# Kernel tuning notes

Measured on AMD Instinct MI355X. Metric: run time of the kernel, lower is better.

## Reference

```python
import jax, jax.numpy as jnp
import numpy as np

B, SEQ, DIM = 2, 2048, 1024
HEADS, DIM_HEAD = 16, 64
INNER = HEADS * DIM_HEAD
SCALE = DIM_HEAD ** -0.5


def rotate_half(x):
    # pair consecutive dims (d r) with r=2: (x1, x2) -> (-x2, x1)
    xp = x.reshape(*x.shape[:-1], -1, 2)
    x1, x2 = xp[..., 0], xp[..., 1]
    return jnp.stack((-x2, x1), axis=-1).reshape(x.shape)


def apply_rotary_emb(freqs, t):
    # freqs: [n, rot_dim] angles; t: [b, h, n, d]
    rot_dim = freqs.shape[-1]
    t_rot, t_pass = t[..., :rot_dim], t[..., rot_dim:]
    t_rot = t_rot * jnp.cos(freqs) + rotate_half(t_rot) * jnp.sin(freqs)
    return jnp.concatenate([t_rot, t_pass], axis=-1)


def setup_inputs() -> dict:
    key = jax.random.key(0)
    ks = jax.random.split(key, 4)
    x = jax.random.normal(ks[0], (B, SEQ, DIM), dtype=jnp.float32)
    mask = jnp.ones((B, SEQ), dtype=bool)
    rotary_pos_emb = jax.random.uniform(ks[1], (SEQ, DIM_HEAD), dtype=jnp.float32)
    Wqkv = jax.random.normal(ks[2], (DIM, 3 * INNER), dtype=jnp.float32) * 0.02
    Wout = jax.random.normal(ks[3], (INNER, DIM), dtype=jnp.float32) * 0.02
    bout = jnp.zeros((DIM,), dtype=jnp.float32)
    return {"x": x, "mask": mask, "rotary_pos_emb": rotary_pos_emb,
            "Wqkv": Wqkv, "Wout": Wout, "bout": bout}


def reference(x, mask, rotary_pos_emb, Wqkv, Wout, bout):
    b, n, _ = x.shape
    qkv = x @ Wqkv                                   # [b, n, 3*inner]
    q, k, v = jnp.split(qkv, 3, axis=-1)

    def to_heads(t):
        return t.reshape(b, n, HEADS, DIM_HEAD).transpose(0, 2, 1, 3)  # [b,h,n,d]

    q, k, v = to_heads(q), to_heads(k), to_heads(v)
    freqs = rotary_pos_emb[:n, :]
    # NB: original applies rotary to q, k AND v
    q = apply_rotary_emb(freqs, q)
    k = apply_rotary_emb(freqs, k)
    v = apply_rotary_emb(freqs, v)
    q = q * SCALE

    dots = jnp.einsum('bhid,bhjd->bhij', q, k)       # [b,h,n,n]
    mask_value = -jnp.finfo(dots.dtype).max
    pad = mask[:, None, None, :]                     # [b,1,1,n] keep where True
    dots = jnp.where(pad, dots, mask_value)
    idx = jnp.arange(n)
    causal = idx[None, :] > idx[:, None]             # j >= i + (j-i+1) with i==j==n
    dots = jnp.where(causal[None, None], mask_value, dots)

    attn = jax.nn.softmax(dots, axis=-1)
    out = jnp.einsum('bhij,bhjd->bhid', attn, v)     # [b,h,n,d]
    out = out.transpose(0, 2, 1, 3).reshape(b, n, INNER)
    return out @ Wout + bout
```

## Files before the change

### kernel.cpp

```cpp
#include <hip/hip_runtime.h>
#include <hip/hip_bf16.h>
#include <stdint.h>

#define DEVI __device__ __forceinline__

typedef __bf16 bf16x8 __attribute__((ext_vector_type(8)));
typedef float f32x4 __attribute__((ext_vector_type(4)));
typedef float f32x16 __attribute__((ext_vector_type(16)));

static constexpr int SEQ = 2048;
static constexpr int DIM = 1024;
static constexpr int HEADS = 16;
static constexpr int NQKV = 3072;
static constexpr int MROWS = 4096;
static constexpr float QSCALE = 0.125f;
static constexpr float LOG2E = 1.4426950408889634f;

DEVI unsigned short f2bf(float f) {
  unsigned int u = __builtin_bit_cast(unsigned int, f);
  u += 0x7FFFu + ((u >> 16) & 1u);
  return (unsigned short)(u >> 16);
}

DEVI bf16x8 ld8(const unsigned short* p) {
  return __builtin_bit_cast(bf16x8, *(const uint4*)p);
}

DEVI f32x4 mfma16(bf16x8 a, bf16x8 b, f32x4 c) {
  return __builtin_amdgcn_mfma_f32_16x16x32_bf16(a, b, c, 0, 0, 0);
}

DEVI f32x16 mfma32(bf16x8 a, bf16x8 b, f32x16 c) {
  return __builtin_amdgcn_mfma_f32_32x32x16_bf16(a, b, c, 0, 0, 0);
}

DEVI void load_lds16(const void* g, void* l) {
  __builtin_amdgcn_global_load_lds((const __attribute__((address_space(1))) void*)g,
                                   (__attribute__((address_space(3))) void*)l,
                                   16, 0, 0);
}

DEVI int swz(int row, int kelem) {
  return row * 64 + (kelem ^ ((row & 7) << 3));
}

DEVI unsigned cvtpk(float lo, float hi) {
  unsigned r;
  asm("v_cvt_pk_bf16_f32 %0, %1, %2" : "=v"(r) : "v"(lo), "v"(hi));
  return r;
}

DEVI void pl32swap(unsigned& a, unsigned& b) {
  asm volatile("v_permlane32_swap_b32 %0, %1" : "+v"(a), "+v"(b));
}
DEVI float xhalf_max(float v) { return fmaxf(v, __shfl_xor(v, 32)); }
DEVI float xhalf_sum(float v) { return v + __shfl_xor(v, 32); }

DEVI void transpose_tile(const float* __restrict__ in, unsigned short* __restrict__ out,
                         int Kd, int Nd, int bx, int by, int tid,
                         unsigned short (*T)[68]) {
  const int n0 = bx * 64, k0 = by * 64;
  const int rr = tid >> 4, cc = (tid & 15) * 4;
#pragma unroll
  for (int p = 0; p < 4; ++p) {
    const int r = p * 16 + rr;
    float4 f = *(const float4*)(in + (size_t)(k0 + r) * Nd + n0 + cc);
    T[r][cc + 0] = f2bf(f.x);
    T[r][cc + 1] = f2bf(f.y);
    T[r][cc + 2] = f2bf(f.z);
    T[r][cc + 3] = f2bf(f.w);
  }
  __syncthreads();
#pragma unroll
  for (int p = 0; p < 4; ++p) {
    const int rn = p * 16 + rr;
    ushort4 v;
    v.x = T[cc + 0][rn];
    v.y = T[cc + 1][rn];
    v.z = T[cc + 2][rn];
    v.w = T[cc + 3][rn];
    *(ushort4*)(out + (size_t)(n0 + rn) * Kd + k0 + cc) = v;
  }
}

__global__ __launch_bounds__(256) void k_prep(
    const float* __restrict__ x, unsigned short* __restrict__ xb,
    const float* __restrict__ rope, float* __restrict__ cosb, float* __restrict__ sinb,
    const float* __restrict__ Wqkv, unsigned short* __restrict__ wqkvt,
    const float* __restrict__ Wout, unsigned short* __restrict__ woutt) {
  __shared__ unsigned short T[64][68];
  const int bid = blockIdx.x, tid = threadIdx.x;
  if (bid < 4096) {
    const int i = bid * 256 + tid;
    float4 f = *(const float4*)(x + (size_t)i * 4);
    ushort4 v;
    v.x = f2bf(f.x); v.y = f2bf(f.y); v.z = f2bf(f.z); v.w = f2bf(f.w);
    *(ushort4*)(xb + (size_t)i * 4) = v;
  } else if (bid < 4608) {
    const int i = (bid - 4096) * 256 + tid;
    float f = rope[i];
    cosb[i] = cosf(f);
    sinb[i] = sinf(f);
  } else if (bid < 5376) {
    const int idx = bid - 4608;
    transpose_tile(Wqkv, wqkvt, DIM, NQKV, idx % 48, idx / 48, tid, T);
  } else {
    const int idx = bid - 5376;
    transpose_tile(Wout, woutt, DIM, DIM, idx % 16, idx / 16, tid, T);
  }
}

DEVI void gemm_mainloop64(const unsigned short* __restrict__ A,
                          const unsigned short* __restrict__ B, int K,
                          int m0, int n0,
                          unsigned short* As, unsigned short* Bs,
                          f32x4 (&acc)[4][4]) {
  const int lane = threadIdx.x & 63;
  const int wid = threadIdx.x >> 6;
  const int wm = wid >> 1, wn = wid & 1;
  const int rsub = lane >> 3;
  const int ksw = ((lane & 7) ^ rsub) * 8;
  for (int kt = 0; kt < K; kt += 64) {
    __syncthreads();
#pragma unroll
    for (int i = 0; i < 4; ++i) {
      const int chunk = wid * 4 + i;
      const int row = chunk * 8 + rsub;
      load_lds16(A + (size_t)(m0 + row) * K + kt + ksw, As + chunk * 512);
      load_lds16(B + (size_t)(n0 + row) * K + kt + ksw, Bs + chunk * 512);
    }
    __syncthreads();
#pragma unroll
    for (int kk = 0; kk < 2; ++kk) {
      bf16x8 af[4], bfv[4];
#pragma unroll
      for (int mi = 0; mi < 4; ++mi)
        af[mi] = ld8(&As[swz(wm * 64 + mi * 16 + (lane & 15),
                             kk * 32 + 8 * (lane >> 4))]);
#pragma unroll
      for (int ni = 0; ni < 4; ++ni)
        bfv[ni] = ld8(&Bs[swz(wn * 64 + ni * 16 + (lane & 15),
                              kk * 32 + 8 * (lane >> 4))]);
#pragma unroll
      for (int mi = 0; mi < 4; ++mi)
#pragma unroll
        for (int ni = 0; ni < 4; ++ni)
          acc[mi][ni] = mfma16(af[mi], bfv[ni], acc[mi][ni]);
    }
  }
}

__global__ __launch_bounds__(512, 1) void k_gemm_qkv(
    const unsigned short* __restrict__ xb, const unsigned short* __restrict__ wt,
    const float* __restrict__ cosb, const float* __restrict__ sinb,
    unsigned short* __restrict__ qb, unsigned short* __restrict__ kb,
    unsigned short* __restrict__ vb) {
  __shared__ __align__(16) unsigned short Ab[2][2][8192];
  __shared__ __align__(16) unsigned short Bb[2][12288];
  const int tid = threadIdx.x, lane = tid & 63, wid = tid >> 6;
  const int wm = wid >> 2, wn = wid & 3;
  const int m0 = blockIdx.x * 256, n0 = blockIdx.y * 192;
  const int la15 = lane & 15, l16 = lane >> 4;
  const int pS0 = tid, pS1 = tid + 512;
  const int sr0 = pS0 >> 3, sr1 = pS1 >> 3;
  const int sc0 = ((pS0 & 7) ^ (sr0 & 7)) * 8, sc1 = ((pS1 & 7) ^ (sr1 & 7)) * 8;
  const int bsr = tid >> 3;
  const int bsc = ((tid & 7) ^ (bsr & 7)) * 8;

  auto stageA = [&](int h, int s) {
    const unsigned short* src = xb + (size_t)(m0 + h * 128) * DIM + s * 64;
    unsigned short* dst = &Ab[s & 1][h][0];
    load_lds16(src + (size_t)sr0 * DIM + sc0, dst + pS0 * 8);
    load_lds16(src + (size_t)sr1 * DIM + sc1, dst + pS1 * 8);
  };
  auto stageB3 = [&](int t, int s) {
    const unsigned short* src = wt + (size_t)(n0 + t * 64 + bsr) * DIM + s * 64;
    load_lds16(src + bsc, &Bb[s & 1][t * 4096] + tid * 8);
  };

  f32x4 acc[8][3] = {};
  stageA(0, 0); stageA(1, 0); stageB3(0, 0); stageB3(1, 0); stageB3(2, 0);
  stageA(0, 1); stageA(1, 1); stageB3(0, 1); stageB3(1, 1); stageB3(2, 1);

#pragma unroll 1
  for (int s = 0; s < 16; ++s) {
    const unsigned short* Ah = &Ab[s & 1][wm][0];
    const unsigned short* Bh = &Bb[s & 1][0];
    const int rb = wn * 48;
    bf16x8 bfr[3][2];
#pragma unroll
    for (int q = 0; q < 4; ++q) {
      if (q == 0) {
        if (s == 0)       asm volatile("s_waitcnt vmcnt(7)" ::: "memory");
        else if (s == 15) asm volatile("s_waitcnt vmcnt(0)" ::: "memory");
        else              asm volatile("s_waitcnt vmcnt(3)" ::: "memory");
        __syncthreads();
      }
      if (q == 2) __syncthreads();
      bf16x8 afr[2][2];
      if (q == 0) {
#pragma unroll
        for (int ni = 0; ni < 3; ++ni)
#pragma unroll
          for (int kk = 0; kk < 2; ++kk)
            bfr[ni][kk] = ld8(&Bh[swz(rb + ni * 16 + la15, kk * 32 + 8 * l16)]);
      }
#pragma unroll
      for (int mi = 0; mi < 2; ++mi)
#pragma unroll
        for (int kk = 0; kk < 2; ++kk)
          afr[mi][kk] = ld8(&Ah[swz(q * 32 + mi * 16 + la15, kk * 32 + 8 * l16)]);
      if (q == 0)      { if (s >= 1 && s + 1 < 16) stageA(0, s + 1); }
      else if (q == 1) { if (s >= 1 && s + 1 < 16) stageA(1, s + 1); }
      else if (q == 2) { if (s + 2 < 16) stageB3(0, s + 2); }
      else             { if (s + 2 < 16) { stageB3(1, s + 2); stageB3(2, s + 2); } }
      asm volatile("s_waitcnt lgkmcnt(0)" ::: "memory");
      __builtin_amdgcn_sched_barrier(0);
      __builtin_amdgcn_s_setprio(1);
#pragma unroll
      for (int kk = 0; kk < 2; ++kk)
#pragma unroll
        for (int mi = 0; mi < 2; ++mi)
#pragma unroll
          for (int ni = 0; ni < 3; ++ni)
            acc[2 * q + mi][ni] = mfma16(afr[mi][kk], bfr[ni][kk], acc[2 * q + mi][ni]);
      __builtin_amdgcn_s_setprio(0);
    }
  }

#pragma unroll
  for (int mq = 0; mq < 8; ++mq) {
#pragma unroll
    for (int ni = 0; ni < 3; ++ni) {
      const int ng = n0 + wn * 48 + ni * 16 + la15;
      const int d = ng & 63;
      const int part = ng >> 10;
      const int h = (ng & 1023) >> 6;
      const int mg0 = m0 + wm * 128 + mq * 16 + 4 * l16;
      const int s0 = mg0 & (SEQ - 1), b = mg0 >> 11;
      const size_t bh = (size_t)(b * HEADS + h);
      if (part == 2) {
        ushort4 vv;
#pragma unroll
        for (int r = 0; r < 4; ++r) {
          const int s = s0 + r;
          float v = acc[mq][ni][r];
          float p = __shfl_xor(v, 1);
          float cv = cosb[(s << 6) + d], sv = sinb[(s << 6) + d];
          float rot = v * cv + ((d & 1) ? p : -p) * sv;
          ((unsigned short*)&vv)[r] = f2bf(rot);
        }
        *(ushort4*)(vb + (bh * 64 + d) * SEQ + s0) = vv;
      } else {
#pragma unroll
        for (int r = 0; r < 4; ++r) {
          const int s = s0 + r;
          float v = acc[mq][ni][r];
          float p = __shfl_xor(v, 1);
          float cv = cosb[(s << 6) + d], sv = sinb[(s << 6) + d];
          float rot = v * cv + ((d & 1) ? p : -p) * sv;
          if (part == 0) {
            qb[(bh * SEQ + s) * 64 + d] = f2bf(rot * (QSCALE * LOG2E));
          } else {
            kb[(bh * SEQ + s) * 64 + d] = f2bf(rot);
          }
        }
      }
    }
  }
}

__global__ __launch_bounds__(256) void k_flash(
    const unsigned short* __restrict__ qb, const unsigned short* __restrict__ kb,
    const unsigned short* __restrict__ vtb, unsigned short* __restrict__ ao) {
  __shared__ __align__(16) unsigned short Ks[2][2][64 * 64];
  __shared__ __align__(16) unsigned short Vt[2][2][64 * 64];
  const int bh = blockIdx.x;
  const int j = blockIdx.y;
  const int tid = threadIdx.x, lane = tid & 63, wid = tid >> 6;
  const int wq = wid >> 1, wk = wid & 1;
  const int la31 = lane & 31, h = lane >> 5;
  const unsigned short* kbh = kb + (size_t)bh * SEQ * 64;
  const unsigned short* vbh = vtb + (size_t)bh * 64 * SEQ;
  const int b = bh >> 4, hh = bh & 15;
  const int sslot = ((lane & 7) ^ (lane >> 3)) * 8;
  float* mrg = (float*)&Ks[0][0][0];
  const int mbase = wq * 2176;

  auto stage = [&](int buf, int t) {
    const int kv0 = t * 64;
#pragma unroll
    for (int i = 0; i < 4; ++i) {
      const int chunk = wq * 4 + i;
      const int row = chunk * 8 + (lane >> 3);
      load_lds16(kbh + ((size_t)(kv0 + row) << 6) + sslot, &Ks[buf][wk][chunk * 512]);
      load_lds16(vbh + (size_t)row * SEQ + kv0 + sslot, &Vt[buf][wk][chunk * 512]);
    }
  };

#pragma unroll 1
  for (int hf = 0; hf < 2; ++hf) {
    const int qt = hf == 0 ? (31 - j) : j;
    const int q0 = qt * 64 + wq * 32;
    const int qr = q0 + la31;
    const unsigned short* qp = qb + ((size_t)bh * SEQ + qr) * 64;
    bf16x8 qf0 = ld8(qp + 0 + 8 * h);
    bf16x8 qf1 = ld8(qp + 16 + 8 * h);
    bf16x8 qf2 = ld8(qp + 32 + 8 * h);
    bf16x8 qf3 = ld8(qp + 48 + 8 * h);

    f32x16 o0 = {}, o1 = {};
    float m = -1e30f, l = 0.f;
    const int nkv = qt + 1;
    const int nst = (nkv + 1) >> 1;

    if (wk < nkv) stage(0, wk);
#pragma unroll 1
    for (int st = 0; st < nst; ++st) {
      const int cur = st & 1;
      const int t = 2 * st + wk;
      __syncthreads();
      { const int tn = 2 * (st + 1) + wk; if (tn < nkv) stage(cur ^ 1, tn); }

      if (t < nkv) {
        const int kv0 = t * 64;
        const unsigned short* Kc = &Ks[cur][wk][0];
        const unsigned short* Vc = &Vt[cur][wk][0];
        f32x16 st0 = {}, st1 = {};
        __builtin_amdgcn_s_setprio(1);
#pragma unroll
        for (int ks = 0; ks < 4; ++ks) {
          bf16x8 qk = (ks == 0) ? qf0 : (ks == 1) ? qf1 : (ks == 2) ? qf2 : qf3;
          st0 = mfma32(ld8(&Kc[swz(la31, 16 * ks + 8 * h)]), qk, st0);
          st1 = mfma32(ld8(&Kc[swz(32 + la31, 16 * ks + 8 * h)]), qk, st1);
        }
        __builtin_amdgcn_s_setprio(0);
        if (kv0 + 63 > q0) {
#pragma unroll
          for (int r = 0; r < 16; ++r) {
            const int kvo = (r & 3) + 8 * (r >> 2) + 4 * h;
            st0[r] = (kv0 + kvo > qr) ? -1e30f : st0[r];
            st1[r] = (kv0 + 32 + kvo > qr) ? -1e30f : st1[r];
          }
        }
        float a8[8];
#pragma unroll
        for (int i = 0; i < 8; ++i)
          a8[i] = fmaxf(fmaxf(st0[i], st0[i + 8]), fmaxf(st1[i], st1[i + 8]));
        float a4_0 = fmaxf(a8[0], a8[4]), a4_1 = fmaxf(a8[1], a8[5]);
        float a4_2 = fmaxf(a8[2], a8[6]), a4_3 = fmaxf(a8[3], a8[7]);
        float pmax = fmaxf(fmaxf(a4_0, a4_1), fmaxf(a4_2, a4_3));
        const bool nor = __all(pmax <= m + 8.f);
        float scl = 1.f;
        if (!nor) {
          const float rowmax = xhalf_max(pmax);
          const float mnew = fmaxf(m, rowmax);
          scl = exp2f(m - mnew);
          m = mnew;
        }
#pragma unroll
        for (int r = 0; r < 16; ++r) {
          st0[r] = exp2f(st0[r] - m);
          st1[r] = exp2f(st1[r] - m);
        }
        float s8[8];
#pragma unroll
        for (int i = 0; i < 8; ++i)
          s8[i] = (st0[i] + st0[i + 8]) + (st1[i] + st1[i + 8]);
        float s4_0 = s8[0] + s8[4], s4_1 = s8[1] + s8[5];
        float s4_2 = s8[2] + s8[6], s4_3 = s8[3] + s8[7];
        float psum = (s4_0 + s4_1) + (s4_2 + s4_3);
        const float rowsum = xhalf_sum(psum);
        if (nor) {
          l += rowsum;
        } else {
          l = l * scl + rowsum;
#pragma unroll
          for (int r = 0; r < 16; ++r) { o0[r] *= scl; o1[r] *= scl; }
        }

        unsigned w0 = cvtpk(st0[0], st0[1]),   w1 = cvtpk(st0[2], st0[3]);
        unsigned w2 = cvtpk(st0[4], st0[5]),   w3 = cvtpk(st0[6], st0[7]);
        unsigned w4 = cvtpk(st0[8], st0[9]),   w5 = cvtpk(st0[10], st0[11]);
        unsigned w6 = cvtpk(st0[12], st0[13]), w7 = cvtpk(st0[14], st0[15]);
        pl32swap(w0, w2); pl32swap(w1, w3); pl32swap(w4, w6); pl32swap(w5, w7);
        const bf16x8 pa0 = __builtin_bit_cast(bf16x8, (uint4){w0, w1, w2, w3});
        const bf16x8 pa1 = __builtin_bit_cast(bf16x8, (uint4){w4, w5, w6, w7});
        unsigned x0 = cvtpk(st1[0], st1[1]),   x1 = cvtpk(st1[2], st1[3]);
        unsigned x2 = cvtpk(st1[4], st1[5]),   x3 = cvtpk(st1[6], st1[7]);
        unsigned x4 = cvtpk(st1[8], st1[9]),   x5 = cvtpk(st1[10], st1[11]);
        unsigned x6 = cvtpk(st1[12], st1[13]), x7 = cvtpk(st1[14], st1[15]);
        pl32swap(x0, x2); pl32swap(x1, x3); pl32swap(x4, x6); pl32swap(x5, x7);
        const bf16x8 pa2 = __builtin_bit_cast(bf16x8, (uint4){x0, x1, x2, x3});
        const bf16x8 pa3 = __builtin_bit_cast(bf16x8, (uint4){x4, x5, x6, x7});

        __builtin_amdgcn_s_setprio(1);
        o0 = mfma32(ld8(&Vc[swz(la31, 0 + 8 * h)]), pa0, o0);
        o0 = mfma32(ld8(&Vc[swz(la31, 16 + 8 * h)]), pa1, o0);
        o0 = mfma32(ld8(&Vc[swz(la31, 32 + 8 * h)]), pa2, o0);
        o0 = mfma32(ld8(&Vc[swz(la31, 48 + 8 * h)]), pa3, o0);
        o1 = mfma32(ld8(&Vc[swz(32 + la31, 0 + 8 * h)]), pa0, o1);
        o1 = mfma32(ld8(&Vc[swz(32 + la31, 16 + 8 * h)]), pa1, o1);
        o1 = mfma32(ld8(&Vc[swz(32 + la31, 32 + 8 * h)]), pa2, o1);
        o1 = mfma32(ld8(&Vc[swz(32 + la31, 48 + 8 * h)]), pa3, o1);
        __builtin_amdgcn_s_setprio(0);
      }
    }

    __syncthreads();
    if (wk == 1) {
#pragma unroll
      for (int s = 0; s < 8; ++s) {
        f32x4 c;
        if (s < 4) { c[0]=o0[4*s]; c[1]=o0[4*s+1]; c[2]=o0[4*s+2]; c[3]=o0[4*s+3]; }
        else       { c[0]=o1[4*(s-4)]; c[1]=o1[4*(s-4)+1]; c[2]=o1[4*(s-4)+2]; c[3]=o1[4*(s-4)+3]; }
        *(f32x4*)&mrg[mbase + lane * 32 + 4 * (s ^ (lane & 7))] = c;
      }
      mrg[mbase + 2048 + lane] = m;
      mrg[mbase + 2112 + lane] = l;
    }
    __syncthreads();
    if (wk == 0) {
      const float m1 = mrg[mbase + 2048 + lane];
      const float l1 = mrg[mbase + 2112 + lane];
      const float mM = fmaxf(m, m1);
      const float sc0 = exp2f(m - mM), sc1 = exp2f(m1 - mM);
      const float lt = l * sc0 + l1 * sc1;
      const float rl = __builtin_amdgcn_rcpf(lt);
      unsigned short* aor = ao + ((size_t)(b * SEQ + qr)) * 1024 + hh * 64;
#pragma unroll
      for (int s = 0; s < 8; ++s) {
        f32x4 c = *(const f32x4*)&mrg[mbase + lane * 32 + 4 * (s ^ (lane & 7))];
        float v0, v1, v2, v3;
        if (s < 4) {
          v0 = (o0[4*s]   * sc0 + c[0] * sc1) * rl;
          v1 = (o0[4*s+1] * sc0 + c[1] * sc1) * rl;
          v2 = (o0[4*s+2] * sc0 + c[2] * sc1) * rl;
          v3 = (o0[4*s+3] * sc0 + c[3] * sc1) * rl;
        } else {
          v0 = (o1[4*(s-4)]   * sc0 + c[0] * sc1) * rl;
          v1 = (o1[4*(s-4)+1] * sc0 + c[1] * sc1) * rl;
          v2 = (o1[4*(s-4)+2] * sc0 + c[2] * sc1) * rl;
          v3 = (o1[4*(s-4)+3] * sc0 + c[3] * sc1) * rl;
        }
        uint2 uv;
        uv.x = cvtpk(v0, v1);
        uv.y = cvtpk(v2, v3);
        *(uint2*)(aor + (s < 4 ? 8 * s : 32 + 8 * (s - 4)) + 4 * h) = uv;
      }
    }
    __syncthreads();
  }
}

__global__ __launch_bounds__(256) void k_gemm_out(
    const unsigned short* __restrict__ ao, const unsigned short* __restrict__ wt,
    const float* __restrict__ bout, float* __restrict__ out) {
  __shared__ __align__(16) unsigned short As[128 * 64];
  __shared__ __align__(16) unsigned short Bs[128 * 64];
  const int m0 = blockIdx.x * 128, n0 = blockIdx.y * 128;
  f32x4 acc[4][4] = {};
  gemm_mainloop64(ao, wt, DIM, m0, n0, As, Bs, acc);
  const int lane = threadIdx.x & 63, wid = threadIdx.x >> 6;
  const int wm = wid >> 1, wn = wid & 1;
#pragma unroll
  for (int mi = 0; mi < 4; ++mi) {
#pragma unroll
    for (int ni = 0; ni < 4; ++ni) {
      const int ng = n0 + wn * 64 + ni * 16 + (lane & 15);
      const float bn = bout[ng];
#pragma unroll
      for (int r = 0; r < 4; ++r) {
        const int mg = m0 + wm * 64 + mi * 16 + 4 * (lane >> 4) + r;
        out[(size_t)mg * DIM + ng] = acc[mi][ni][r] + bn;
      }
    }
  }
}

extern "C" void kernel_launch(void* const* d_in, const int* in_sizes, int n_in,
                              void* d_out, int out_size, void* d_ws, size_t ws_size,
                              hipStream_t stream) {
  const float* x    = (const float*)d_in[0];
  const float* rope = (const float*)d_in[2];
  const float* Wqkv = (const float*)d_in[3];
  const float* Wout = (const float*)d_in[4];
  const float* bout = (const float*)d_in[5];
  float* out = (float*)d_out;

  char* ws = (char*)d_ws;
  unsigned short* xb    = (unsigned short*)(ws + 0);
  unsigned short* wqkvt = (unsigned short*)(ws + 8388608);
  unsigned short* woutt = (unsigned short*)(ws + 14680064);
  float*          cosb  = (float*)(ws + 16777216);
  float*          sinb  = (float*)(ws + 17301504);
  unsigned short* qbuf  = (unsigned short*)(ws + 17825792);
  unsigned short* kbuf  = (unsigned short*)(ws + 26214400);
  unsigned short* vbuf  = (unsigned short*)(ws + 34603008);
  unsigned short* aob   = (unsigned short*)(ws + 42991616);

  k_prep<<<5632, 256, 0, stream>>>(x, xb, rope, cosb, sinb, Wqkv, wqkvt, Wout, woutt);
  k_gemm_qkv<<<dim3(16, 16), 512, 0, stream>>>(xb, wqkvt, cosb, sinb,
                                               qbuf, kbuf, vbuf);
  k_flash<<<dim3(32, 16), 256, 0, stream>>>(qbuf, kbuf, vbuf, aob);
  k_gemm_out<<<dim3(MROWS / 128, DIM / 128), 256, 0, stream>>>(aob, woutt, bout, out);
}
```

Measured before the change: 125.1 us.

## Split paired causal q-tiles into separate blocks and single-buffer V tiles

The flash kernel no longer processes two q-tiles (a long and a short one) per block; the grid doubles to 32x32 with one q-tile per block, ordered longest first. V is now staged into a single LDS buffer, loaded at the start of each step and consumed after a second barrier, which shrinks LDS use per block. This raises the number of blocks and may improve occupancy, but loses the explicit load balancing of the pairing and adds an extra barrier per KV step.

```diff
diff --git a/kernel.cpp b/kernel.cpp
--- a/kernel.cpp
+++ b/kernel.cpp
@@ -273,10 +273,10 @@
 __global__ __launch_bounds__(256) void k_flash(
     const unsigned short* __restrict__ qb, const unsigned short* __restrict__ kb,
     const unsigned short* __restrict__ vtb, unsigned short* __restrict__ ao) {
-  __shared__ __align__(16) unsigned short Ks[2][2][64 * 64];
-  __shared__ __align__(16) unsigned short Vt[2][2][64 * 64];
+  __shared__ __align__(16) unsigned short Ks[2][2][4096];
+  __shared__ __align__(16) unsigned short Vt[2][4096];
   const int bh = blockIdx.x;
-  const int j = blockIdx.y;
+  const int qt = 31 - blockIdx.y;
   const int tid = threadIdx.x, lane = tid & 63, wid = tid >> 6;
   const int wq = wid >> 1, wk = wid & 1;
   const int la31 = lane & 31, h = lane >> 5;
@@ -287,169 +287,176 @@
   float* mrg = (float*)&Ks[0][0][0];
   const int mbase = wq * 2176;
 
-  auto stage = [&](int buf, int t) {
+  auto stageK = [&](int buf, int t) {
     const int kv0 = t * 64;
 #pragma unroll
     for (int i = 0; i < 4; ++i) {
       const int chunk = wq * 4 + i;
       const int row = chunk * 8 + (lane >> 3);
       load_lds16(kbh + ((size_t)(kv0 + row) << 6) + sslot, &Ks[buf][wk][chunk * 512]);
-      load_lds16(vbh + (size_t)row * SEQ + kv0 + sslot, &Vt[buf][wk][chunk * 512]);
     }
   };
-
+  auto stageV = [&](int t) {
+    const int kv0 = t * 64;
+#pragma unroll
+    for (int i = 0; i < 4; ++i) {
+      const int chunk = wq * 4 + i;
+      const int row = chunk * 8 + (lane >> 3);
+      load_lds16(vbh + (size_t)row * SEQ + kv0 + sslot, &Vt[wk][chunk * 512]);
+    }
+  };
+
+  const int q0 = qt * 64 + wq * 32;
+  const int qr = q0 + la31;
+  const unsigned short* qp = qb + ((size_t)bh * SEQ + qr) * 64;
+  bf16x8 qf0 = ld8(qp + 0 + 8 * h);
+  bf16x8 qf1 = ld8(qp + 16 + 8 * h);
+  bf16x8 qf2 = ld8(qp + 32 + 8 * h);
+  bf16x8 qf3 = ld8(qp + 48 + 8 * h);
+
+  f32x16 o0 = {}, o1 = {};
+  float m = -1e30f, l = 0.f;
+  const int nkv = qt + 1;
+  const int nst = (nkv + 1) >> 1;
+
+  if (wk < nkv) stageK(0, wk);
 #pragma unroll 1
-  for (int hf = 0; hf < 2; ++hf) {
-    const int qt = hf == 0 ? (31 - j) : j;
-    const int q0 = qt * 64 + wq * 32;
-    const int qr = q0 + la31;
-    const unsigned short* qp = qb + ((size_t)bh * SEQ + qr) * 64;
-    bf16x8 qf0 = ld8(qp + 0 + 8 * h);
-    bf16x8 qf1 = ld8(qp + 16 + 8 * h);
-    bf16x8 qf2 = ld8(qp + 32 + 8 * h);
-    bf16x8 qf3 = ld8(qp + 48 + 8 * h);
-
-    f32x16 o0 = {}, o1 = {};
-    float m = -1e30f, l = 0.f;
-    const int nkv = qt + 1;
-    const int nst = (nkv + 1) >> 1;
-
-    if (wk < nkv) stage(0, wk);
-#pragma unroll 1
-    for (int st = 0; st < nst; ++st) {
-      const int cur = st & 1;
-      const int t = 2 * st + wk;
-      __syncthreads();
-      { const int tn = 2 * (st + 1) + wk; if (tn < nkv) stage(cur ^ 1, tn); }
-
-      if (t < nkv) {
-        const int kv0 = t * 64;
-        const unsigned short* Kc = &Ks[cur][wk][0];
-        const unsigned short* Vc = &Vt[cur][wk][0];
-        f32x16 st0 = {}, st1 = {};
-        __builtin_amdgcn_s_setprio(1);
-#pragma unroll
-        for (int ks = 0; ks < 4; ++ks) {
-          bf16x8 qk = (ks == 0) ? qf0 : (ks == 1) ? qf1 : (ks == 2) ? qf2 : qf3;
-          st0 = mfma32(ld8(&Kc[swz(la31, 16 * ks + 8 * h)]), qk, st0);
-          st1 = mfma32(ld8(&Kc[swz(32 + la31, 16 * ks + 8 * h)]), qk, st1);
+  for (int st = 0; st < nst; ++st) {
+    const int cur = st & 1;
+    const int t = 2 * st + wk;
+    const bool live = (t < nkv);
+    __syncthreads();
+    if (live) stageV(t);
+    { const int tn = 2 * (st + 1) + wk; if (tn < nkv) stageK(cur ^ 1, tn); }
+
+    f32x16 st0 = {}, st1 = {};
+    bf16x8 pa0, pa1, pa2, pa3;
+    if (live) {
+      const int kv0 = t * 64;
+      const unsigned short* Kc = &Ks[cur][wk][0];
+      __builtin_amdgcn_s_setprio(1);
+#pragma unroll
+      for (int ks = 0; ks < 4; ++ks) {
+        bf16x8 qk = (ks == 0) ? qf0 : (ks == 1) ? qf1 : (ks == 2) ? qf2 : qf3;
+        st0 = mfma32(ld8(&Kc[swz(la31, 16 * ks + 8 * h)]), qk, st0);
+        st1 = mfma32(ld8(&Kc[swz(32 + la31, 16 * ks + 8 * h)]), qk, st1);
+      }
+      __builtin_amdgcn_s_setprio(0);
+      if (kv0 + 63 > q0) {
+#pragma unroll
+        for (int r = 0; r < 16; ++r) {
+          const int kvo = (r & 3) + 8 * (r >> 2) + 4 * h;
+          st0[r] = (kv0 + kvo > qr) ? -1e30f : st0[r];
+          st1[r] = (kv0 + 32 + kvo > qr) ? -1e30f : st1[r];
         }
-        __builtin_amdgcn_s_setprio(0);
-        if (kv0 + 63 > q0) {
-#pragma unroll
-          for (int r = 0; r < 16; ++r) {
-            const int kvo = (r & 3) + 8 * (r >> 2) + 4 * h;
-            st0[r] = (kv0 + kvo > qr) ? -1e30f : st0[r];
-            st1[r] = (kv0 + 32 + kvo > qr) ? -1e30f : st1[r];
-          }
-        }
-        float a8[8];
-#pragma unroll
-        for (int i = 0; i < 8; ++i)
-          a8[i] = fmaxf(fmaxf(st0[i], st0[i + 8]), fmaxf(st1[i], st1[i + 8]));
-        float a4_0 = fmaxf(a8[0], a8[4]), a4_1 = fmaxf(a8[1], a8[5]);
-        float a4_2 = fmaxf(a8[2], a8[6]), a4_3 = fmaxf(a8[3], a8[7]);
-        float pmax = fmaxf(fmaxf(a4_0, a4_1), fmaxf(a4_2, a4_3));
-        const bool nor = __all(pmax <= m + 8.f);
-        float scl = 1.f;
-        if (!nor) {
-          const float rowmax = xhalf_max(pmax);
-          const float mnew = fmaxf(m, rowmax);
-          scl = exp2f(m - mnew);
-          m = mnew;
-        }
-#pragma unroll
-        for (int r = 0; r < 16; ++r) {
-          st0[r] = exp2f(st0[r] - m);
-          st1[r] = exp2f(st1[r] - m);
-        }
-        float s8[8];
-#pragma unroll
-        for (int i = 0; i < 8; ++i)
-          s8[i] = (st0[i] + st0[i + 8]) + (st1[i] + st1[i + 8]);
-        float s4_0 = s8[0] + s8[4], s4_1 = s8[1] + s8[5];
-        float s4_2 = s8[2] + s8[6], s4_3 = s8[3] + s8[7];
-        float psum = (s4_0 + s4_1) + (s4_2 + s4_3);
-        const float rowsum = xhalf_sum(psum);
-        if (nor) {
-          l += rowsum;
-        } else {
-          l = l * scl + rowsum;
-#pragma unroll
-          for (int r = 0; r < 16; ++r) { o0[r] *= scl; o1[r] *= scl; }
-        }
-
-        unsigned w0 = cvtpk(st0[0], st0[1]),   w1 = cvtpk(st0[2], st0[3]);
-        unsigned w2 = cvtpk(st0[4], st0[5]),   w3 = cvtpk(st0[6], st0[7]);
-        unsigned w4 = cvtpk(st0[8], st0[9]),   w5 = cvtpk(st0[10], st0[11]);
-        unsigned w6 = cvtpk(st0[12], st0[13]), w7 = cvtpk(st0[14], st0[15]);
-        pl32swap(w0, w2); pl32swap(w1, w3); pl32swap(w4, w6); pl32swap(w5, w7);
-        const bf16x8 pa0 = __builtin_bit_cast(bf16x8, (uint4){w0, w1, w2, w3});
-        const bf16x8 pa1 = __builtin_bit_cast(bf16x8, (uint4){w4, w5, w6, w7});
-        unsigned x0 = cvtpk(st1[0], st1[1]),   x1 = cvtpk(st1[2], st1[3]);
-        unsigned x2 = cvtpk(st1[4], st1[5]),   x3 = cvtpk(st1[6], st1[7]);
-        unsigned x4 = cvtpk(st1[8], st1[9]),   x5 = cvtpk(st1[10], st1[11]);
-        unsigned x6 = cvtpk(st1[12], st1[13]), x7 = cvtpk(st1[14], st1[15]);
-        pl32swap(x0, x2); pl32swap(x1, x3); pl32swap(x4, x6); pl32swap(x5, x7);
-        const bf16x8 pa2 = __builtin_bit_cast(bf16x8, (uint4){x0, x1, x2, x3});
-        const bf16x8 pa3 = __builtin_bit_cast(bf16x8, (uint4){x4, x5, x6, x7});
-
-        __builtin_amdgcn_s_setprio(1);
-        o0 = mfma32(ld8(&Vc[swz(la31, 0 + 8 * h)]), pa0, o0);
-        o0 = mfma32(ld8(&Vc[swz(la31, 16 + 8 * h)]), pa1, o0);
-        o0 = mfma32(ld8(&Vc[swz(la31, 32 + 8 * h)]), pa2, o0);
-        o0 = mfma32(ld8(&Vc[swz(la31, 48 + 8 * h)]), pa3, o0);
-        o1 = mfma32(ld8(&Vc[swz(32 + la31, 0 + 8 * h)]), pa0, o1);
-        o1 = mfma32(ld8(&Vc[swz(32 + la31, 16 + 8 * h)]), pa1, o1);
-        o1 = mfma32(ld8(&Vc[swz(32 + la31, 32 + 8 * h)]), pa2, o1);
-        o1 = mfma32(ld8(&Vc[swz(32 + la31, 48 + 8 * h)]), pa3, o1);
-        __builtin_amdgcn_s_setprio(0);
-      }
-    }
-
+      }
+      float a8[8];
+#pragma unroll
+      for (int i = 0; i < 8; ++i)
+        a8[i] = fmaxf(fmaxf(st0[i], st0[i + 8]), fmaxf(st1[i], st1[i + 8]));
+      float a4_0 = fmaxf(a8[0], a8[4]), a4_1 = fmaxf(a8[1], a8[5]);
+      float a4_2 = fmaxf(a8[2], a8[6]), a4_3 = fmaxf(a8[3], a8[7]);
+      float pmax = fmaxf(fmaxf(a4_0, a4_1), fmaxf(a4_2, a4_3));
+      const bool nor = __all(pmax <= m + 8.f);
+      float scl = 1.f;
+      if (!nor) {
+        const float rowmax = xhalf_max(pmax);
+        const float mnew = fmaxf(m, rowmax);
+        scl = exp2f(m - mnew);
+        m = mnew;
+      }
+#pragma unroll
+      for (int r = 0; r < 16; ++r) {
+        st0[r] = exp2f(st0[r] - m);
+        st1[r] = exp2f(st1[r] - m);
+      }
+      float s8[8];
+#pragma unroll
+      for (int i = 0; i < 8; ++i)
+        s8[i] = (st0[i] + st0[i + 8]) + (st1[i] + st1[i + 8]);
+      float s4_0 = s8[0] + s8[4], s4_1 = s8[1] + s8[5];
+      float s4_2 = s8[2] + s8[6], s4_3 = s8[3] + s8[7];
+      float psum = (s4_0 + s4_1) + (s4_2 + s4_3);
+      const float rowsum = xhalf_sum(psum);
+      if (nor) {
+        l += rowsum;
+      } else {
+        l = l * scl + rowsum;
+#pragma unroll
+        for (int r = 0; r < 16; ++r) { o0[r] *= scl; o1[r] *= scl; }
+      }
+      unsigned w0 = cvtpk(st0[0], st0[1]),   w1 = cvtpk(st0[2], st0[3]);
+      unsigned w2 = cvtpk(st0[4], st0[5]),   w3 = cvtpk(st0[6], st0[7]);
+      unsigned w4 = cvtpk(st0[8], st0[9]),   w5 = cvtpk(st0[10], st0[11]);
+      unsigned w6 = cvtpk(st0[12], st0[13]), w7 = cvtpk(st0[14], st0[15]);
+      pl32swap(w0, w2); pl32swap(w1, w3); pl32swap(w4, w6); pl32swap(w5, w7);
+      pa0 = __builtin_bit_cast(bf16x8, (uint4){w0, w1, w2, w3});
+      pa1 = __builtin_bit_cast(bf16x8, (uint4){w4, w5, w6, w7});
+      unsigned x0 = cvtpk(st1[0], st1[1]),   x1 = cvtpk(st1[2], st1[3]);
+      unsigned x2 = cvtpk(st1[4], st1[5]),   x3 = cvtpk(st1[6], st1[7]);
+      unsigned x4 = cvtpk(st1[8], st1[9]),   x5 = cvtpk(st1[10], st1[11]);
+      unsigned x6 = cvtpk(st1[12], st1[13]), x7 = cvtpk(st1[14], st1[15]);
+      pl32swap(x0, x2); pl32swap(x1, x3); pl32swap(x4, x6); pl32swap(x5, x7);
+      pa2 = __builtin_bit_cast(bf16x8, (uint4){x0, x1, x2, x3});
+      pa3 = __builtin_bit_cast(bf16x8, (uint4){x4, x5, x6, x7});
+    }
     __syncthreads();
-    if (wk == 1) {
-#pragma unroll
-      for (int s = 0; s < 8; ++s) {
-        f32x4 c;
-        if (s < 4) { c[0]=o0[4*s]; c[1]=o0[4*s+1]; c[2]=o0[4*s+2]; c[3]=o0[4*s+3]; }
-        else       { c[0]=o1[4*(s-4)]; c[1]=o1[4*(s-4)+1]; c[2]=o1[4*(s-4)+2]; c[3]=o1[4*(s-4)+3]; }
-        *(f32x4*)&mrg[mbase + lane * 32 + 4 * (s ^ (lane & 7))] = c;
-      }
-      mrg[mbase + 2048 + lane] = m;
-      mrg[mbase + 2112 + lane] = l;
-    }
-    __syncthreads();
-    if (wk == 0) {
-      const float m1 = mrg[mbase + 2048 + lane];
-      const float l1 = mrg[mbase + 2112 + lane];
-      const float mM = fmaxf(m, m1);
-      const float sc0 = exp2f(m - mM), sc1 = exp2f(m1 - mM);
-      const float lt = l * sc0 + l1 * sc1;
-      const float rl = __builtin_amdgcn_rcpf(lt);
-      unsigned short* aor = ao + ((size_t)(b * SEQ + qr)) * 1024 + hh * 64;
-#pragma unroll
-      for (int s = 0; s < 8; ++s) {
-        f32x4 c = *(const f32x4*)&mrg[mbase + lane * 32 + 4 * (s ^ (lane & 7))];
-        float v0, v1, v2, v3;
-        if (s < 4) {
-          v0 = (o0[4*s]   * sc0 + c[0] * sc1) * rl;
-          v1 = (o0[4*s+1] * sc0 + c[1] * sc1) * rl;
-          v2 = (o0[4*s+2] * sc0 + c[2] * sc1) * rl;
-          v3 = (o0[4*s+3] * sc0 + c[3] * sc1) * rl;
-        } else {
-          v0 = (o1[4*(s-4)]   * sc0 + c[0] * sc1) * rl;
-          v1 = (o1[4*(s-4)+1] * sc0 + c[1] * sc1) * rl;
-          v2 = (o1[4*(s-4)+2] * sc0 + c[2] * sc1) * rl;
-          v3 = (o1[4*(s-4)+3] * sc0 + c[3] * sc1) * rl;
-        }
-        uint2 uv;
-        uv.x = cvtpk(v0, v1);
-        uv.y = cvtpk(v2, v3);
-        *(uint2*)(aor + (s < 4 ? 8 * s : 32 + 8 * (s - 4)) + 4 * h) = uv;
-      }
-    }
-    __syncthreads();
+    if (live) {
+      const unsigned short* Vc = &Vt[wk][0];
+      __builtin_amdgcn_s_setprio(1);
+      o0 = mfma32(ld8(&Vc[swz(la31, 0 + 8 * h)]), pa0, o0);
+      o0 = mfma32(ld8(&Vc[swz(la31, 16 + 8 * h)]), pa1, o0);
+      o0 = mfma32(ld8(&Vc[swz(la31, 32 + 8 * h)]), pa2, o0);
+      o0 = mfma32(ld8(&Vc[swz(la31, 48 + 8 * h)]), pa3, o0);
+      o1 = mfma32(ld8(&Vc[swz(32 + la31, 0 + 8 * h)]), pa0, o1);
+      o1 = mfma32(ld8(&Vc[swz(32 + la31, 16 + 8 * h)]), pa1, o1);
+      o1 = mfma32(ld8(&Vc[swz(32 + la31, 32 + 8 * h)]), pa2, o1);
+      o1 = mfma32(ld8(&Vc[swz(32 + la31, 48 + 8 * h)]), pa3, o1);
+      __builtin_amdgcn_s_setprio(0);
+    }
+  }
+
+  __syncthreads();
+  if (wk == 1) {
+#pragma unroll
+    for (int s = 0; s < 8; ++s) {
+      f32x4 c;
+      if (s < 4) { c[0]=o0[4*s]; c[1]=o0[4*s+1]; c[2]=o0[4*s+2]; c[3]=o0[4*s+3]; }
+      else       { c[0]=o1[4*(s-4)]; c[1]=o1[4*(s-4)+1]; c[2]=o1[4*(s-4)+2]; c[3]=o1[4*(s-4)+3]; }
+      *(f32x4*)&mrg[mbase + lane * 32 + 4 * (s ^ (lane & 7))] = c;
+    }
+    mrg[mbase + 2048 + lane] = m;
+    mrg[mbase + 2112 + lane] = l;
+  }
+  __syncthreads();
+  if (wk == 0) {
+    const float m1 = mrg[mbase + 2048 + lane];
+    const float l1 = mrg[mbase + 2112 + lane];
+    const float mM = fmaxf(m, m1);
+    const float sc0 = exp2f(m - mM), sc1 = exp2f(m1 - mM);
+    const float lt = l * sc0 + l1 * sc1;
+    const float rl = __builtin_amdgcn_rcpf(lt);
+    unsigned short* aor = ao + ((size_t)(b * SEQ + qr)) * 1024 + hh * 64;
+#pragma unroll
+    for (int s = 0; s < 8; ++s) {
+      f32x4 c = *(const f32x4*)&mrg[mbase + lane * 32 + 4 * (s ^ (lane & 7))];
+      float v0, v1, v2, v3;
+      if (s < 4) {
+        v0 = (o0[4*s]   * sc0 + c[0] * sc1) * rl;
+        v1 = (o0[4*s+1] * sc0 + c[1] * sc1) * rl;
+        v2 = (o0[4*s+2] * sc0 + c[2] * sc1) * rl;
+        v3 = (o0[4*s+3] * sc0 + c[3] * sc1) * rl;
+      } else {
+        v0 = (o1[4*(s-4)]   * sc0 + c[0] * sc1) * rl;
+        v1 = (o1[4*(s-4)+1] * sc0 + c[1] * sc1) * rl;
+        v2 = (o1[4*(s-4)+2] * sc0 + c[2] * sc1) * rl;
+        v3 = (o1[4*(s-4)+3] * sc0 + c[3] * sc1) * rl;
+      }
+      uint2 uv;
+      uv.x = cvtpk(v0, v1);
+      uv.y = cvtpk(v2, v3);
+      *(uint2*)(aor + (s < 4 ? 8 * s : 32 + 8 * (s - 4)) + 4 * h) = uv;
+    }
   }
 }
 
@@ -502,6 +509,6 @@
   k_prep<<<5632, 256, 0, stream>>>(x, xb, rope, cosb, sinb, Wqkv, wqkvt, Wout, woutt);
   k_gemm_qkv<<<dim3(16, 16), 512, 0, stream>>>(xb, wqkvt, cosb, sinb,
                                                qbuf, kbuf, vbuf);
-  k_flash<<<dim3(32, 16), 256, 0, stream>>>(qbuf, kbuf, vbuf, aob);
+  k_flash<<<dim3(32, 32), 256, 0, stream>>>(qbuf, kbuf, vbuf, aob);
   k_gemm_out<<<dim3(MROWS / 128, DIM / 128), 256, 0, stream>>>(aob, woutt, bout, out);
 }
```

New measurement: 120.9 us. -3.3%, faster.
